# Kernel tuning notes

Hardware: AMD Instinct MI355X
Metric: run time of the kernel (lower is better)

The kernel has to match this reference:

```python
import jax, jax.numpy as jnp
import numpy as np

# --- static config (mirrors init_kwargs) ---
B, C, H, W = 32, 128, 16, 16
V = 8192                 # vocab_size
PNS = (1, 2, 4, 8, 16)   # v_patch_nums; last one == H == W
BETA = 0.25
RATIO = 0.5              # Phi resi_ratio
K_PHI = 4                # share_quant_resi: number of Phi conv blocks
_TICKS = np.linspace(1.0 / (3 * K_PHI), 1.0 - 1.0 / (3 * K_PHI), K_PHI)


def setup_inputs() -> dict:
    key = jax.random.key(0)
    k1, k2, k3 = jax.random.split(key, 3)
    f_BChw = jax.random.normal(k1, (B, C, H, W), jnp.float32)
    embedding = jax.random.normal(k2, (V, C), jnp.float32) * 0.5
    phi_w = jax.random.normal(k3, (K_PHI, C, C, 3, 3), jnp.float32) * 0.02
    phi_b = jnp.zeros((K_PHI, C), jnp.float32)
    return {"f_BChw": f_BChw, "embedding": embedding, "phi_w": phi_w, "phi_b": phi_b}


def _avg_pool(x, pn):
    # F.interpolate(mode='area') with divisible sizes == exact block mean
    b, c, h, w = x.shape
    return x.reshape(b, c, pn, h // pn, pn, w // pn).mean(axis=(3, 5))


def _phi(h, w, b):
    # Phi: x*(1-r) + conv3x3(x)*r
    y = jax.lax.conv_general_dilated(
        h, w, window_strides=(1, 1), padding='SAME',
        dimension_numbers=('NCHW', 'OIHW', 'NCHW'))
    y = y + b[None, :, None, None]
    return h * (1.0 - RATIO) + y * RATIO


def reference(f_BChw, embedding, phi_w, phi_b):
    f = f_BChw
    f_rest = jax.lax.stop_gradient(f)       # f_BChw.detach().clone()
    f_hat = jnp.zeros_like(f)
    SN = len(PNS)
    loss = jnp.float32(0.0)
    e_sq = jnp.sum(embedding ** 2, axis=1)  # [V]
    for si, pn in enumerate(PNS):
        rest = f_rest if si == SN - 1 else _avg_pool(f_rest, pn)
        rest_NC = rest.transpose(0, 2, 3, 1).reshape(-1, C)          # [B*pn*pn, C]
        # squared euclidean distance to codebook, argmin over V
        d = (jnp.sum(rest_NC ** 2, axis=1, keepdims=True) + e_sq
             - 2.0 * rest_NC @ embedding.T)                           # [N, V]
        idx = jnp.argmin(d, axis=1)                                   # [N]
        h = embedding[idx].reshape(B, pn, pn, C).transpose(0, 3, 1, 2)  # [B,C,pn,pn]
        if si != SN - 1:
            h = jax.image.resize(h, (B, C, H, W), method='cubic')     # bicubic upsample
        kphi = int(np.argmin(np.abs(_TICKS - si / (SN - 1))))
        h = _phi(h, phi_w[kphi], phi_b[kphi])
        f_hat = f_hat + h
        f_rest = f_rest - h
        loss = loss + (BETA * jnp.mean((jax.lax.stop_gradient(f_hat) - f) ** 2)
                       + jnp.mean((f_hat - jax.lax.stop_gradient(f)) ** 2))
    loss = loss / SN
    # straight-through: f_hat.data - f.detach() + f
    f_hat_out = jax.lax.stop_gradient(f_hat - f) + f
    return f_hat_out, loss
```

## Files before the change

kernel.cpp:

```cpp
#include <hip/hip_runtime.h>
#include <math.h>

#define CC   128
#define HH   16
#define WW   16
#define BB   32
#define VV   8192
#define NELEM (BB*CC*HH*WW)

typedef short short8 __attribute__((ext_vector_type(8)));
typedef float floatx4 __attribute__((ext_vector_type(4)));

#define CSTR 136

typedef __attribute__((address_space(1))) void as1_void;
typedef __attribute__((address_space(3))) void as3_void;

__device__ __forceinline__ void gl_lds16(const void* g, void* l) {
    __builtin_amdgcn_global_load_lds((as1_void*)g, (as3_void*)l, 16, 0, 0);
}

__device__ __forceinline__ uint32_t pack_hilo(float x) {
    uint32_t u = __float_as_uint(x);
    uint32_t hb = (u + 0x7fffu + ((u >> 16) & 1u)) & 0xffff0000u;
    float hf = __uint_as_float(hb);
    float lo = x - hf;
    uint32_t ul = __float_as_uint(lo);
    uint32_t lb = ((ul + 0x7fffu + ((ul >> 16) & 1u)) >> 16) & 0xffffu;
    return hb | lb;
}

__global__ void esq_pack(const float* __restrict__ emb, float* __restrict__ esq,
                         short* __restrict__ ephi, short* __restrict__ eplo,
                         float* __restrict__ lacc) {
    int t = blockIdx.x * 256 + threadIdx.x;
    int v = t >> 4, g = t & 15;
    const float* row = emb + (size_t)v * CC + g * 8;
    float4 a = *(const float4*)row;
    float4 b = *(const float4*)(row + 4);
    float s = a.x*a.x + a.y*a.y + a.z*a.z + a.w*a.w
            + b.x*b.x + b.y*b.y + b.z*b.z + b.w*b.w;
    s += __shfl_xor(s, 1, 64);
    s += __shfl_xor(s, 2, 64);
    s += __shfl_xor(s, 4, 64);
    s += __shfl_xor(s, 8, 64);
    if (g == 0) esq[v] = s;
    float vals[8] = {a.x, a.y, a.z, a.w, b.x, b.y, b.z, b.w};
    short hs[8], ls[8];
#pragma unroll
    for (int j = 0; j < 8; j++) {
        uint32_t u = pack_hilo(vals[j]);
        hs[j] = (short)(u >> 16);
        ls[j] = (short)(u & 0xffffu);
    }
    int vt = v >> 7, vr = v & 127;
    int vh = vr >> 6, tj = (vr >> 4) & 3, r15 = vr & 15;
    int kc = g >> 2, quad = g & 3;
    size_t off = (size_t)vt * 16384 + (size_t)((kc * 8 + vh * 4 + tj) * 64 + quad * 16 + r15) * 8;
    *(short8*)(ephi + off) = *(short8*)hs;
    *(short8*)(eplo + off) = *(short8*)ls;
    if (t == 0) lacc[0] = 0.f;
}

__global__ void prepack_w(const float* __restrict__ pw, short* __restrict__ Whi,
                          short* __restrict__ Wlo) {
    int id = blockIdx.x * 256 + threadIdx.x;
    int ci = id & 127, cout = (id >> 7) & 127, kp = id >> 14;
    const float* src = pw + ((size_t)(kp * CC + cout) * CC + ci) * 9;
#pragma unroll
    for (int kk = 0; kk < 9; kk++) {
        uint32_t u = pack_hilo(src[kk]);
        size_t o = ((size_t)(kp * 9 + kk) * CC + cout) * CC + ci;
        Whi[o] = (short)(u >> 16);
        Wlo[o] = (short)(u & 0xffffu);
    }
}

template <bool FIRSTP>
__global__ void pool_pack(const float* __restrict__ f, const float* __restrict__ fh,
                          short* __restrict__ rh, short* __restrict__ rl, int pn) {
    int id = blockIdx.x * 256 + threadIdx.x;
    int c = id % CC;
    int n = id / CC;
    int px = n % pn;
    int py = (n / pn) % pn;
    int b  = n / (pn * pn);
    int s  = HH / pn;
    size_t o = (((size_t)b * CC + c) * HH + py * s) * WW + px * s;
    float acc = 0.f;
    for (int dy = 0; dy < s; dy++)
        for (int dx = 0; dx < s; dx++)
            acc += FIRSTP ? f[o + dy * WW + dx] : (f[o + dy * WW + dx] - fh[o + dy * WW + dx]);
    uint32_t u = pack_hilo(acc * (1.f / (float)(s * s)));
    rh[id] = (short)(u >> 16);
    rl[id] = (short)(u & 0xffffu);
}

__global__ __launch_bounds__(512, 4)
void dist_mfma(const short* __restrict__ rphi, const short* __restrict__ rplo,
               const short* __restrict__ ephi, const short* __restrict__ eplo,
               const float* __restrict__ esq,
               float* __restrict__ pbD, int* __restrict__ pbI,
               int N, int vtPB) {
    __shared__ short Bs[2][2][8192];
    __shared__ float EsqL[1024];

    const int tid  = threadIdx.x;
    const int wave = tid >> 6, ln = tid & 63;
    const int quad = ln >> 4, l15 = ln & 15;
    const int qq = wave & 3, vh = wave >> 2;
    const int qb0 = blockIdx.x * 128;
    const int vslices = gridDim.y;
    const int vt0 = blockIdx.y * vtPB;
    const int nsteps = vtPB * 2;

#define STAGE_STEP(buf_, s_) do {                                                    \
        const int vt_ = vt0 + ((s_) >> 1);                                           \
        const int hf_ = (s_) & 1;                                                    \
        _Pragma("unroll")                                                            \
        for (int i_ = 0; i_ < 2; i_++) {                                             \
            const int ck_ = wave * 2 + i_;                                           \
            const int kc_ = ck_ >> 2, g_ = ck_ & 3;                                  \
            const size_t so_ = (size_t)vt_ * 32768 +                                 \
                               (size_t)(kc_ * 8 + hf_ * 4 + g_) * 1024;              \
            gl_lds16((const char*)ephi + so_ + ln * 16, (char*)&Bs[(buf_)][0][0] + ck_ * 1024); \
            gl_lds16((const char*)eplo + so_ + ln * 16, (char*)&Bs[(buf_)][1][0] + ck_ * 1024); \
        } } while (0)

    STAGE_STEP(0, 0);
    {
        int echunks = (vtPB * 512 + 1023) >> 10;
        if (wave < echunks)
            gl_lds16((const char*)(esq + vt0 * 128) + wave * 1024 + ln * 16,
                     (char*)EsqL + wave * 1024);
    }

    short8 av[2][4], aw[2][4];
#pragma unroll
    for (int ti = 0; ti < 2; ti++) {
        const size_t arow = (size_t)(qb0 + qq * 32 + ti * 16 + l15) * CC + quad * 8;
#pragma unroll
        for (int kc = 0; kc < 4; kc++) {
            av[ti][kc] = *(const short8*)(rphi + arow + kc * 32);
            aw[ti][kc] = *(const short8*)(rplo + arow + kc * 32);
        }
    }
    __builtin_amdgcn_sched_barrier(0);
    asm volatile("s_waitcnt vmcnt(0)" ::: "memory");
    __builtin_amdgcn_sched_barrier(0);
    __builtin_amdgcn_s_barrier();
    __builtin_amdgcn_sched_barrier(0);

    float bD[2][4];
    int   bI[2][4];
#pragma unroll
    for (int ti = 0; ti < 2; ti++)
#pragma unroll
        for (int r = 0; r < 4; r++) { bD[ti][r] = INFINITY; bI[ti][r] = 0; }

    int cur = 0;
    for (int s = 0; s < nsteps; s++) {
        if (s + 1 < nsteps) STAGE_STEP(cur ^ 1, s + 1);
        __builtin_amdgcn_sched_barrier(0);

        floatx4 acc[2][2];
        floatx4 z = {0.f, 0.f, 0.f, 0.f};
#pragma unroll
        for (int ti = 0; ti < 2; ti++)
#pragma unroll
            for (int tj = 0; tj < 2; tj++) acc[ti][tj] = z;

        const short* Bh = &Bs[cur][0][0];
        const short* Bl = &Bs[cur][1][0];
#pragma unroll
        for (int kc = 0; kc < 4; kc++) {
            short8 bh[2], bl[2];
#pragma unroll
            for (int tj = 0; tj < 2; tj++) {
                const int ck = kc * 4 + vh * 2 + tj;
                bh[tj] = *(const short8*)(Bh + ck * 512 + ln * 8);
                bl[tj] = *(const short8*)(Bl + ck * 512 + ln * 8);
            }
            __builtin_amdgcn_s_setprio(1);
#pragma unroll
            for (int tj = 0; tj < 2; tj++)
#pragma unroll
                for (int ti = 0; ti < 2; ti++)
                    acc[ti][tj] = __builtin_amdgcn_mfma_f32_16x16x32_bf16(av[ti][kc], bh[tj], acc[ti][tj], 0, 0, 0);
#pragma unroll
            for (int tj = 0; tj < 2; tj++)
#pragma unroll
                for (int ti = 0; ti < 2; ti++)
                    acc[ti][tj] = __builtin_amdgcn_mfma_f32_16x16x32_bf16(aw[ti][kc], bh[tj], acc[ti][tj], 0, 0, 0);
#pragma unroll
            for (int tj = 0; tj < 2; tj++)
#pragma unroll
                for (int ti = 0; ti < 2; ti++)
                    acc[ti][tj] = __builtin_amdgcn_mfma_f32_16x16x32_bf16(av[ti][kc], bl[tj], acc[ti][tj], 0, 0, 0);
#pragma unroll
            for (int tj = 0; tj < 2; tj++)
#pragma unroll
                for (int ti = 0; ti < 2; ti++)
                    acc[ti][tj] = __builtin_amdgcn_mfma_f32_16x16x32_bf16(aw[ti][kc], bl[tj], acc[ti][tj], 0, 0, 0);
            __builtin_amdgcn_s_setprio(0);
        }

        const int v0 = (vt0 + (s >> 1)) * 128 + (s & 1) * 64;
#pragma unroll
        for (int tj = 0; tj < 2; tj++) {
            int vg = v0 + vh * 32 + tj * 16 + l15;
            float ev = EsqL[s * 64 + vh * 32 + tj * 16 + l15];
#pragma unroll
            for (int ti = 0; ti < 2; ti++)
#pragma unroll
                for (int r = 0; r < 4; r++) {
                    float d = fmaf(-2.f, acc[ti][tj][r], ev);
                    if (d < bD[ti][r]) { bD[ti][r] = d; bI[ti][r] = vg; }
                }
        }

        __builtin_amdgcn_sched_barrier(0);
        asm volatile("s_waitcnt vmcnt(0)" ::: "memory");
        __builtin_amdgcn_sched_barrier(0);
        __builtin_amdgcn_s_barrier();
        __builtin_amdgcn_sched_barrier(0);
        cur ^= 1;
    }
#undef STAGE_STEP

#pragma unroll
    for (int ti = 0; ti < 2; ti++)
#pragma unroll
        for (int r = 0; r < 4; r++) {
            float d = bD[ti][r];
            int   v = bI[ti][r];
#pragma unroll
            for (int m = 1; m <= 8; m <<= 1) {
                float od = __shfl_xor(d, m, 64);
                int   ov = __shfl_xor(v, m, 64);
                if (od < d || (od == d && ov < v)) { d = od; v = ov; }
            }
            if (l15 == 0) {
                int q = qb0 + qq * 32 + ti * 16 + quad * 4 + r;
                if (q < N) {
                    size_t o = (size_t)q * (vslices * 2) + blockIdx.y * 2 + vh;
                    pbD[o] = d;
                    pbI[o] = v;
                }
            }
        }
}

__device__ __forceinline__ float cubic_k(float x) {
    if (x <= 1.f) return (1.5f * x - 2.5f) * x * x + 1.f;
    if (x < 2.f)  return ((-0.5f * x + 2.5f) * x - 4.f) * x + 2.f;
    return 0.f;
}

template <int PN>
__global__ __launch_bounds__(256)
void upsample_pack(const float* __restrict__ emb,
                   const float* __restrict__ pbD, const int* __restrict__ pbI, int vsplit,
                   short* __restrict__ hhi, short* __restrict__ hlo,
                   float* __restrict__ hfp) {
    const int t = threadIdx.x;
    const int x = t & 15, y = t >> 4;
    const int b = blockIdx.x >> 4;
    const int c0 = (blockIdx.x & 15) * 8;

    float val[8];

    if constexpr (PN == 16) {
        int q = b * 256 + t;
        float bd = pbD[(size_t)q * vsplit];
        int   bi = pbI[(size_t)q * vsplit];
        for (int j = 1; j < vsplit; j++) {
            float d  = pbD[(size_t)q * vsplit + j];
            int   i2 = pbI[(size_t)q * vsplit + j];
            if (d < bd || (d == bd && i2 < bi)) { bd = d; bi = i2; }
        }
        float4 v0 = *(const float4*)(emb + (size_t)bi * CC + c0);
        float4 v1 = *(const float4*)(emb + (size_t)bi * CC + c0 + 4);
        val[0]=v0.x; val[1]=v0.y; val[2]=v0.z; val[3]=v0.w;
        val[4]=v1.x; val[5]=v1.y; val[6]=v1.z; val[7]=v1.w;
    } else {
        constexpr int NQ = PN * PN;
        constexpr int KK = 256 / NQ;
        __shared__ int idxL[NQ];
        __shared__ float S[NQ][8];
        __shared__ float prd[256];
        __shared__ int   pri[256];

        {
            const int qi = t & (NQ - 1);
            const int kk = t / NQ;
            float bd = INFINITY; int bi = 0;
            for (int j = kk; j < vsplit; j += KK) {
                float d  = pbD[(size_t)(b * NQ + qi) * vsplit + j];
                int   i2 = pbI[(size_t)(b * NQ + qi) * vsplit + j];
                if (d < bd || (d == bd && i2 < bi)) { bd = d; bi = i2; }
            }
            prd[t] = bd; pri[t] = bi;
        }
        __syncthreads();
        if (t < 64) {
            float d = prd[t]; int v = pri[t];
            for (int p = t + 64; p < 256; p += 64) {
                float d2 = prd[p]; int v2 = pri[p];
                if (d2 < d || (d2 == d && v2 < v)) { d = d2; v = v2; }
            }
#pragma unroll
            for (int m = NQ; m < 64; m <<= 1) {
                float d2 = __shfl_xor(d, m, 64);
                int   v2 = __shfl_xor(v, m, 64);
                if (d2 < d || (d2 == d && v2 < v)) { d = d2; v = v2; }
            }
            if (t < NQ) idxL[t] = v;
        }
        __syncthreads();
        if (t < NQ) {
            float4 v0 = *(const float4*)(emb + (size_t)idxL[t] * CC + c0);
            float4 v1 = *(const float4*)(emb + (size_t)idxL[t] * CC + c0 + 4);
            S[t][0]=v0.x; S[t][1]=v0.y; S[t][2]=v0.z; S[t][3]=v0.w;
            S[t][4]=v1.x; S[t][5]=v1.y; S[t][6]=v1.z; S[t][7]=v1.w;
        }
        __syncthreads();

        const float sc = (float)PN / 16.f;
        float sy = (y + 0.5f) * sc - 0.5f;
        float sx = (x + 0.5f) * sc - 0.5f;
        int iy0 = (int)floorf(sy) - 1;
        int ix0 = (int)floorf(sx) - 1;
        float wy[4], wx[4];
        float ssy = 0.f, ssx = 0.f;
#pragma unroll
        for (int k = 0; k < 4; k++) {
            int iy = iy0 + k, ix = ix0 + k;
            float a = (iy >= 0 && iy < PN) ? cubic_k(fabsf(sy - (float)iy)) : 0.f;
            float bb = (ix >= 0 && ix < PN) ? cubic_k(fabsf(sx - (float)ix)) : 0.f;
            wy[k] = a; ssy += a;
            wx[k] = bb; ssx += bb;
        }
        float ry = 1.f / ssy, rx = 1.f / ssx;
#pragma unroll
        for (int k = 0; k < 4; k++) { wy[k] *= ry; wx[k] *= rx; }

#pragma unroll
        for (int j = 0; j < 8; j++) val[j] = 0.f;
#pragma unroll
        for (int k4 = 0; k4 < 4; k4++) {
            int iy = iy0 + k4;
            if (iy < 0 || iy >= PN) continue;
#pragma unroll
            for (int j4 = 0; j4 < 4; j4++) {
                int ix = ix0 + j4;
                if (ix < 0 || ix >= PN) continue;
                float w = wy[k4] * wx[j4];
                const float* sp = S[iy * PN + ix];
#pragma unroll
                for (int j = 0; j < 8; j++) val[j] = fmaf(w, sp[j], val[j]);
            }
        }
    }

    short hs[8], ls[8];
#pragma unroll
    for (int j = 0; j < 8; j++) {
        uint32_t u = pack_hilo(val[j]);
        hs[j] = (short)(u >> 16);
        ls[j] = (short)(u & 0xffffu);
    }
    size_t ho = ((size_t)(b * 18 + y + 1) * 18 + (x + 1)) * CC + c0;
    *(short8*)(hhi + ho) = *(short8*)hs;
    *(short8*)(hlo + ho) = *(short8*)ls;
#pragma unroll
    for (int j = 0; j < 8; j++)
        hfp[((size_t)b * CC + c0 + j) * 256 + t] = val[j];
}

template <bool FIRST>
__global__ __launch_bounds__(256)
void conv_mfma(const short* __restrict__ Whi, const short* __restrict__ Wlo,
               const short* __restrict__ hhi, const short* __restrict__ hlo,
               const float* __restrict__ hfp, const float* __restrict__ pb,
               const float* __restrict__ f, float* __restrict__ f_hat,
               float* __restrict__ lacc, int kphi) {
    __shared__ short Bsh[64 * CSTR];
    __shared__ short Bsl[64 * CSTR];
    __shared__ float red[2][16][65];
    __shared__ float lred[2];

    const int t = threadIdx.x;
    const int wave = t >> 6, lane = t & 63;
    const int quad = lane >> 4, l15 = lane & 15;
    const int pxg = wave & 1, kh = wave >> 1;
    const int cH = blockIdx.x & 1;
    const int pc = blockIdx.x >> 1;
    const int b = pc >> 3;
    const int pxbase = (pc & 7) * 32;
    const int pa = pxbase + pxg * 16 + l15;
    const int ya = pa >> 4, xa = pa & 15;

    floatx4 acc[4];
    floatx4 z = {0.f, 0.f, 0.f, 0.f};
#pragma unroll
    for (int nt = 0; nt < 4; nt++) acc[nt] = z;

    const int srow = t >> 4, scol = (t & 15) * 8;
    short8 rh[4], rl[4];
    {
        const short* gh = Whi + ((size_t)(kphi * 9 + 0) * CC + cH * 64) * CC;
        const short* gl = Wlo + ((size_t)(kphi * 9 + 0) * CC + cH * 64) * CC;
#pragma unroll
        for (int i = 0; i < 4; i++) {
            rh[i] = *(const short8*)(gh + (srow + i * 16) * CC + scol);
            rl[i] = *(const short8*)(gl + (srow + i * 16) * CC + scol);
        }
    }

    for (int kk = 0; kk < 9; kk++) {
        __syncthreads();
#pragma unroll
        for (int i = 0; i < 4; i++) {
            *(short8*)&Bsh[(srow + i * 16) * CSTR + scol] = rh[i];
            *(short8*)&Bsl[(srow + i * 16) * CSTR + scol] = rl[i];
        }
        __syncthreads();

        if (kk < 8) {
            const short* gh = Whi + ((size_t)(kphi * 9 + kk + 1) * CC + cH * 64) * CC;
            const short* gl = Wlo + ((size_t)(kphi * 9 + kk + 1) * CC + cH * 64) * CC;
#pragma unroll
            for (int i = 0; i < 4; i++) {
                rh[i] = *(const short8*)(gh + (srow + i * 16) * CC + scol);
                rl[i] = *(const short8*)(gl + (srow + i * 16) * CC + scol);
            }
        }

        const int ky = kk / 3, kx = kk % 3;
        const size_t aoff = ((size_t)(b * 18 + ya + ky) * 18 + (xa + kx)) * CC + quad * 8;
#pragma unroll
        for (int i2 = 0; i2 < 2; i2++) {
            const int cic = kh * 2 + i2;
            short8 ah = *(const short8*)(hhi + aoff + cic * 32);
            short8 al = *(const short8*)(hlo + aoff + cic * 32);
#pragma unroll
            for (int nt = 0; nt < 4; nt++) {
                short8 bh = *(const short8*)&Bsh[(nt * 16 + l15) * CSTR + cic * 32 + quad * 8];
                short8 bl = *(const short8*)&Bsl[(nt * 16 + l15) * CSTR + cic * 32 + quad * 8];
                acc[nt] = __builtin_amdgcn_mfma_f32_16x16x32_bf16(ah, bh, acc[nt], 0, 0, 0);
                acc[nt] = __builtin_amdgcn_mfma_f32_16x16x32_bf16(al, bh, acc[nt], 0, 0, 0);
                acc[nt] = __builtin_amdgcn_mfma_f32_16x16x32_bf16(ah, bl, acc[nt], 0, 0, 0);
            }
        }
    }

    __syncthreads();
    if (kh == 1) {
#pragma unroll
        for (int nt = 0; nt < 4; nt++)
#pragma unroll
            for (int r = 0; r < 4; r++)
                red[pxg][quad * 4 + r][nt * 16 + l15] = acc[nt][r];
    }
    __syncthreads();

    if (kh == 0) {
        const int pe = pxbase + pxg * 16 + quad * 4;
        float lsum = 0.f;
#pragma unroll
        for (int nt = 0; nt < 4; nt++) {
            int cout = cH * 64 + nt * 16 + l15;
            float bias = pb[kphi * CC + cout];
            size_t gi = ((size_t)b * CC + cout) * 256 + pe;
            float4 h4  = *(const float4*)(hfp + gi);
            float4 f4  = *(const float4*)(f + gi);
            float4 fh4 = FIRST ? make_float4(0.f, 0.f, 0.f, 0.f) : *(const float4*)(f_hat + gi);
            float c0 = acc[nt][0] + red[pxg][quad * 4 + 0][nt * 16 + l15] + bias;
            float c1 = acc[nt][1] + red[pxg][quad * 4 + 1][nt * 16 + l15] + bias;
            float c2 = acc[nt][2] + red[pxg][quad * 4 + 2][nt * 16 + l15] + bias;
            float c3 = acc[nt][3] + red[pxg][quad * 4 + 3][nt * 16 + l15] + bias;
            float o0 = fh4.x + 0.5f * h4.x + 0.5f * c0;
            float o1 = fh4.y + 0.5f * h4.y + 0.5f * c1;
            float o2 = fh4.z + 0.5f * h4.z + 0.5f * c2;
            float o3 = fh4.w + 0.5f * h4.w + 0.5f * c3;
            *(float4*)(f_hat + gi) = make_float4(o0, o1, o2, o3);
            float d0 = o0 - f4.x, d1 = o1 - f4.y, d2 = o2 - f4.z, d3 = o3 - f4.w;
            lsum += d0*d0 + d1*d1 + d2*d2 + d3*d3;
        }
#pragma unroll
        for (int off = 32; off; off >>= 1) lsum += __shfl_down(lsum, off, 64);
        if (lane == 0) lred[pxg] = lsum;
    }
    __syncthreads();
    if (t == 0) atomicAdd(lacc, lred[0] + lred[1]);
}

__global__ void finalize_kernel(const float* __restrict__ lacc, float* __restrict__ out_loss) {
    *out_loss = lacc[0] * (0.25f / (float)NELEM);
}

extern "C" void kernel_launch(void* const* d_in, const int* in_sizes, int n_in,
                              void* d_out, int out_size, void* d_ws, size_t ws_size,
                              hipStream_t stream) {
    const float* f   = (const float*)d_in[0];
    const float* emb = (const float*)d_in[1];
    const float* pw  = (const float*)d_in[2];
    const float* pb  = (const float*)d_in[3];
    float* out = (float*)d_out;

    uint32_t* w32 = (uint32_t*)d_ws;
    short* rphi = (short*)(w32);
    short* rplo = (short*)(w32 + 524288);
    short* ephi = (short*)(w32 + 1048576);
    short* eplo = (short*)(w32 + 1572864);
    short* Whi  = (short*)(w32 + 2097152);
    short* Wlo  = (short*)(w32 + 2392064);
    short* hhi  = (short*)(w32 + 2686976);
    short* hlo  = (short*)(w32 + 3350528);
    float* hfp  = (float*)(w32 + 4014080);
    float* esq  = (float*)(w32 + 5062656);
    float* pbD  = (float*)(w32 + 5070848);
    int*   pbI  = (int*)  (w32 + 5332992);
    float* lacc = (float*)(w32 + 5595136);

    hipMemsetAsync(hhi, 0, (size_t)2 * 1327104 * sizeof(short), stream);

    esq_pack<<<512, 256, 0, stream>>>(emb, esq, ephi, eplo, lacc);
    prepack_w<<<256, 256, 0, stream>>>(pw, Whi, Wlo);

    double start = 1.0 / 12.0;
    double stop  = 1.0 - 1.0 / 12.0;
    double step  = (stop - start) / 3.0;
    double ticks[4] = {start, 1.0 * step + start, 2.0 * step + start, stop};

    const int pns[5]    = {1, 2, 4, 8, 16};
    const int qb5[5]    = {1, 1, 4, 16, 64};
    const int vs5[5]    = {64, 64, 64, 32, 8};
    const int vtPB5[5]  = {1, 1, 1, 2, 8};

    for (int si = 0; si < 5; si++) {
        int pn = pns[si];
        int N  = BB * pn * pn;
        double tt = (double)si / 4.0;
        int kphi = 0;
        double bd = fabs(ticks[0] - tt);
        for (int i = 1; i < 4; i++) {
            double d = fabs(ticks[i] - tt);
            if (d < bd) { bd = d; kphi = i; }
        }

        if (si == 0) pool_pack<true><<<(N * CC) / 256, 256, 0, stream>>>(f, out, rphi, rplo, pn);
        else         pool_pack<false><<<(N * CC) / 256, 256, 0, stream>>>(f, out, rphi, rplo, pn);

        dim3 dgrid(qb5[si], vs5[si]);
        dist_mfma<<<dgrid, 512, 0, stream>>>(rphi, rplo, ephi, eplo, esq, pbD, pbI, N, vtPB5[si]);

        int vsplit = vs5[si] * 2;
        switch (pn) {
            case 1:  upsample_pack<1><<<512, 256, 0, stream>>>(emb, pbD, pbI, vsplit, hhi, hlo, hfp); break;
            case 2:  upsample_pack<2><<<512, 256, 0, stream>>>(emb, pbD, pbI, vsplit, hhi, hlo, hfp); break;
            case 4:  upsample_pack<4><<<512, 256, 0, stream>>>(emb, pbD, pbI, vsplit, hhi, hlo, hfp); break;
            case 8:  upsample_pack<8><<<512, 256, 0, stream>>>(emb, pbD, pbI, vsplit, hhi, hlo, hfp); break;
            default: upsample_pack<16><<<512, 256, 0, stream>>>(emb, pbD, pbI, vsplit, hhi, hlo, hfp); break;
        }

        if (si == 0) conv_mfma<true><<<512, 256, 0, stream>>>(Whi, Wlo, hhi, hlo, hfp, pb, f, out, lacc, kphi);
        else         conv_mfma<false><<<512, 256, 0, stream>>>(Whi, Wlo, hhi, hlo, hfp, pb, f, out, lacc, kphi);
    }

    finalize_kernel<<<1, 1, 0, stream>>>(lacc, out + NELEM);
}
```

Before: 433.3 us.

## Specialize pool kernel per scale and split codebook finer for small scales

The area-pool kernel becomes a template per patch size. For coarse scales, several threads cooperate on each output using float4 loads and a wave shuffle reduction, replacing one thread serially summing up to 256 strided values. The distance kernel's vocabulary split now works in 64-code steps, so the first three scales can use 128 slices and the last two can take more steps per block. The goal is more parallelism on the latency-bound small scales, at the cost of more partial results for the upsample kernel to reduce.

```diff
diff --git a/kernel.cpp b/kernel.cpp
--- a/kernel.cpp
+++ b/kernel.cpp
@@ -76,24 +76,67 @@
     }
 }
 
-template <bool FIRSTP>
-__global__ void pool_pack(const float* __restrict__ f, const float* __restrict__ fh,
-                          short* __restrict__ rh, short* __restrict__ rl, int pn) {
-    int id = blockIdx.x * 256 + threadIdx.x;
-    int c = id % CC;
-    int n = id / CC;
-    int px = n % pn;
-    int py = (n / pn) % pn;
-    int b  = n / (pn * pn);
-    int s  = HH / pn;
-    size_t o = (((size_t)b * CC + c) * HH + py * s) * WW + px * s;
-    float acc = 0.f;
-    for (int dy = 0; dy < s; dy++)
-        for (int dx = 0; dx < s; dx++)
-            acc += FIRSTP ? f[o + dy * WW + dx] : (f[o + dy * WW + dx] - fh[o + dy * WW + dx]);
-    uint32_t u = pack_hilo(acc * (1.f / (float)(s * s)));
-    rh[id] = (short)(u >> 16);
-    rl[id] = (short)(u & 0xffffu);
+template <int PN, bool FIRSTP>
+__global__ __launch_bounds__(256)
+void pool_pack(const float* __restrict__ f, const float* __restrict__ fh,
+               short* __restrict__ rh, short* __restrict__ rl) {
+    const int tid = threadIdx.x;
+    const int gid = blockIdx.x * 256 + tid;
+
+    if constexpr (PN == 16) {
+        int c = gid % CC;
+        int n = gid / CC;
+        int px = n % 16, py = (n / 16) % 16, b = n / 256;
+        size_t o = (((size_t)b * CC + c) * HH + py) * WW + px;
+        float acc = FIRSTP ? f[o] : (f[o] - fh[o]);
+        uint32_t u = pack_hilo(acc);
+        rh[gid] = (short)(u >> 16);
+        rl[gid] = (short)(u & 0xffffu);
+        return;
+    } else if constexpr (PN == 8) {
+        int c = gid & 127;
+        int n = gid >> 7;
+        int px = n & 7, py = (n >> 3) & 7, b = n >> 6;
+        size_t o = (((size_t)b * CC + c) * HH + py * 2) * WW + px * 2;
+        float acc = 0.f;
+        acc += FIRSTP ? f[o]      : (f[o]      - fh[o]);
+        acc += FIRSTP ? f[o + 1]  : (f[o + 1]  - fh[o + 1]);
+        acc += FIRSTP ? f[o + 16] : (f[o + 16] - fh[o + 16]);
+        acc += FIRSTP ? f[o + 17] : (f[o + 17] - fh[o + 17]);
+        uint32_t u = pack_hilo(acc * 0.25f);
+        rh[gid] = (short)(u >> 16);
+        rl[gid] = (short)(u & 0xffffu);
+        return;
+    } else {
+        constexpr int T = (PN == 1) ? 64 : (PN == 2) ? 16 : 4;
+        const int out = gid / T;
+        const int sub = tid & (T - 1);
+        const int c = out & 127;
+        const int n = out >> 7;
+        const int px = n % PN, py = (n / PN) % PN, b = n / (PN * PN);
+        constexpr int S = 16 / PN;
+        const int rowsPerT = (T * 4) / S;
+        const int row = sub / (S / 4);
+        const int col4 = (sub % (S / 4)) * 4;
+        size_t o = (((size_t)b * CC + c) * HH + py * S + row) * WW + px * S + col4;
+        float4 a = *(const float4*)(f + o);
+        float sum;
+        if (FIRSTP) {
+            sum = ((a.x + a.y) + a.z) + a.w;
+            sum = a.x; sum += a.y; sum += a.z; sum += a.w;
+        } else {
+            float4 h = *(const float4*)(fh + o);
+            sum = (a.x - h.x); sum += (a.y - h.y); sum += (a.z - h.z); sum += (a.w - h.w);
+        }
+#pragma unroll
+        for (int m = 1; m < T; m <<= 1) sum += __shfl_xor(sum, m, 64);
+        if (sub == 0) {
+            uint32_t u = pack_hilo(sum * (1.f / (float)(S * S)));
+            rh[out] = (short)(u >> 16);
+            rl[out] = (short)(u & 0xffffu);
+        }
+        (void)rowsPerT;
+    }
 }
 
 __global__ __launch_bounds__(512, 4)
@@ -101,7 +144,7 @@
                const short* __restrict__ ephi, const short* __restrict__ eplo,
                const float* __restrict__ esq,
                float* __restrict__ pbD, int* __restrict__ pbI,
-               int N, int vtPB) {
+               int N, int st64) {
     __shared__ short Bs[2][2][8192];
     __shared__ float EsqL[1024];
 
@@ -111,12 +154,12 @@
     const int qq = wave & 3, vh = wave >> 2;
     const int qb0 = blockIdx.x * 128;
     const int vslices = gridDim.y;
-    const int vt0 = blockIdx.y * vtPB;
-    const int nsteps = vtPB * 2;
+    const int v64b = blockIdx.y * st64;
+    const int nsteps = st64;
 
 #define STAGE_STEP(buf_, s_) do {                                                    \
-        const int vt_ = vt0 + ((s_) >> 1);                                           \
-        const int hf_ = (s_) & 1;                                                    \
+        const int h_  = v64b + (s_);                                                 \
+        const int vt_ = h_ >> 1, hf_ = h_ & 1;                                       \
         _Pragma("unroll")                                                            \
         for (int i_ = 0; i_ < 2; i_++) {                                             \
             const int ck_ = wave * 2 + i_;                                           \
@@ -129,9 +172,9 @@
 
     STAGE_STEP(0, 0);
     {
-        int echunks = (vtPB * 512 + 1023) >> 10;
+        int echunks = (st64 * 256 + 1023) >> 10;
         if (wave < echunks)
-            gl_lds16((const char*)(esq + vt0 * 128) + wave * 1024 + ln * 16,
+            gl_lds16((const char*)(esq + v64b * 64) + wave * 1024 + ln * 16,
                      (char*)EsqL + wave * 1024);
     }
 
@@ -205,7 +248,7 @@
             __builtin_amdgcn_s_setprio(0);
         }
 
-        const int v0 = (vt0 + (s >> 1)) * 128 + (s & 1) * 64;
+        const int v0 = (v64b + s) * 64;
 #pragma unroll
         for (int tj = 0; tj < 2; tj++) {
             int vg = v0 + vh * 32 + tj * 16 + l15;
@@ -536,8 +579,9 @@
 
     const int pns[5]    = {1, 2, 4, 8, 16};
     const int qb5[5]    = {1, 1, 4, 16, 64};
-    const int vs5[5]    = {64, 64, 64, 32, 8};
-    const int vtPB5[5]  = {1, 1, 1, 2, 8};
+    const int vs5[5]    = {128, 128, 128, 32, 8};
+    const int st5[5]    = {1, 1, 1, 4, 16};
+    const int pgrid5[5] = {1024, 1024, 1024, 1024, 4096};
 
     for (int si = 0; si < 5; si++) {
         int pn = pns[si];
@@ -550,11 +594,16 @@
             if (d < bd) { bd = d; kphi = i; }
         }
 
-        if (si == 0) pool_pack<true><<<(N * CC) / 256, 256, 0, stream>>>(f, out, rphi, rplo, pn);
-        else         pool_pack<false><<<(N * CC) / 256, 256, 0, stream>>>(f, out, rphi, rplo, pn);
+        switch (pn) {
+            case 1:  pool_pack<1,  true ><<<pgrid5[si], 256, 0, stream>>>(f, out, rphi, rplo); break;
+            case 2:  pool_pack<2,  false><<<pgrid5[si], 256, 0, stream>>>(f, out, rphi, rplo); break;
+            case 4:  pool_pack<4,  false><<<pgrid5[si], 256, 0, stream>>>(f, out, rphi, rplo); break;
+            case 8:  pool_pack<8,  false><<<pgrid5[si], 256, 0, stream>>>(f, out, rphi, rplo); break;
+            default: pool_pack<16, false><<<pgrid5[si], 256, 0, stream>>>(f, out, rphi, rplo); break;
+        }
 
         dim3 dgrid(qb5[si], vs5[si]);
-        dist_mfma<<<dgrid, 512, 0, stream>>>(rphi, rplo, ephi, eplo, esq, pbD, pbI, N, vtPB5[si]);
+        dist_mfma<<<dgrid, 512, 0, stream>>>(rphi, rplo, ephi, eplo, esq, pbD, pbI, N, st5[si]);
 
         int vsplit = vs5[si] * 2;
         switch (pn) {
```

Measured after the change: 392.7 us. -9.4%, faster.
